# Kernel tuning notes

Measured on AMD Instinct MI355X. Metric: run time of the kernel, lower is better.

## Reference

```python
import jax, jax.numpy as jnp
import numpy as np

EPS = float(np.finfo(np.float64).eps)  # np.finfo(float).eps as in torch combine


def setup_inputs() -> dict:
    key = jax.random.key(0)
    ks = jax.random.split(key, 4)
    B, E, D_in, D_h, D_out = 4096, 8, 768, 2048, 768
    return {
        "x": jax.random.normal(ks[0], (B, D_in), dtype=jnp.float32),
        "w_gate": jax.random.normal(ks[1], (D_in, E), dtype=jnp.float32) * 0.02,
        "W1": jax.random.normal(ks[2], (E, D_in, D_h), dtype=jnp.float32) * (1.0 / np.sqrt(D_in)),
        "b1": jnp.zeros((E, D_h), dtype=jnp.float32),
        "W2": jax.random.normal(ks[3], (E, D_h, D_out), dtype=jnp.float32) * (1.0 / np.sqrt(D_h)),
        "b2": jnp.zeros((E, D_out), dtype=jnp.float32),
        "k": 2,
    }


def _cv_squared(v):
    # torch .var() is unbiased (ddof=1)
    return jnp.var(v, ddof=1) / (jnp.mean(v) ** 2 + 1e-10)


def _top_k_gates(logits, k):
    B, E = logits.shape
    top_vals, top_idx = jax.lax.top_k(logits, k)        # [B, k]
    top_gates = jax.nn.softmax(top_vals, axis=1)        # softmax over the k kept logits
    gates = jnp.zeros((B, E), logits.dtype).at[jnp.arange(B)[:, None], top_idx].set(top_gates)
    return gates


def reference(x, w_gate, W1, b1, W2, b2, k):
    # --- gating (eval path: noiseless clean logits, softmax gating) ---
    logits = x @ w_gate                                  # [B, E]
    gates = _top_k_gates(logits, k)                      # [B, E], sparse (k nonzeros/row)
    # --- per-expert MLP: Linear -> gelu -> Linear -> log_softmax ---
    # Dense grouped compute over experts; gate==0 terms contribute nothing in combine.
    h = jax.nn.gelu(jnp.einsum('bi,eih->beh', x, W1) + b1[None])      # [B, E, Dh]
    lo = jax.nn.log_softmax(jnp.einsum('beh,eho->beo', h, W2) + b2[None], axis=-1)  # [B, E, Do]
    # --- combine: exp, weight by gates, scatter-add, eps-clamp, log ---
    combined = jnp.einsum('be,beo->bo', gates, jnp.exp(lo))           # [B, Do]
    y = jnp.log(jnp.where(combined == 0, EPS, combined))
    # --- load-balancing aux loss (eval: load = count of nonzero gates) ---
    importance = gates.sum(0)
    load = (gates > 0).sum(0).astype(jnp.float32)
    loss = 0.01 * (_cv_squared(importance) + _cv_squared(load))
    return y, loss
```

## Files before the change

### kernel.cpp

```cpp
#include <hip/hip_runtime.h>
#include <hip/hip_bf16.h>
#include <math.h>

typedef __hip_bfloat16 bf16;
typedef short v8s __attribute__((ext_vector_type(8)));
typedef float v4f __attribute__((ext_vector_type(4)));

#define B_TOK 4096
#define E_EXP 8
#define D_IN  768
#define D_H   2048
#define D_OUT 768
#define MAXT  72

__device__ __forceinline__ void gl_lds16(const bf16* g, bf16* l) {
  __builtin_amdgcn_global_load_lds(
      (const __attribute__((address_space(1))) unsigned int*)g,
      (__attribute__((address_space(3))) unsigned int*)l, 16, 0, 0);
}

__global__ __launch_bounds__(256)
void prep_kernel(const float* __restrict__ x, const float* __restrict__ wg,
                 const float* __restrict__ W1, const float* __restrict__ W2,
                 bf16* __restrict__ W1t, bf16* __restrict__ W2t,
                 bf16* __restrict__ xb, float* __restrict__ gates,
                 int* __restrict__ tidx) {
  __shared__ bf16 tile[64][72];
  const int b = blockIdx.x;
  const int t = threadIdx.x;
  if (b < 6144) {
    const float* W; bf16* Wt; int K, N, kb, nb, e;
    if (b < 3072) {
      W = W1; Wt = W1t; K = D_IN; N = D_H;
      e = b / 384; int rem = b % 384; kb = rem % 12; nb = rem / 12;
    } else {
      int c = b - 3072;
      W = W2; Wt = W2t; K = D_H; N = D_OUT;
      e = c / 384; int rem = c % 384; kb = rem % 32; nb = rem / 32;
    }
    const int k0 = kb * 64, n0 = nb * 64;
    const int w = t >> 6, l = t & 63;
    const int a = l & 3, kl = l >> 2;
    const float* Wp = W + (size_t)e * K * N;
    #pragma unroll
    for (int p = 0; p < 4; ++p) {
      int k_loc = p * 16 + kl;
      int nb4 = w * 16 + a * 4;
      float4 v = *(const float4*)(Wp + (size_t)(k0 + k_loc) * N + n0 + nb4);
      float vv[4] = {v.x, v.y, v.z, v.w};
      #pragma unroll
      for (int i = 0; i < 4; ++i) {
        int n_loc = nb4 + i;
        int phys = (k_loc >> 3) ^ ((n_loc >> 2) & 7);
        tile[n_loc][phys * 8 + (k_loc & 7)] = __float2bfloat16(vv[i]);
      }
    }
    __syncthreads();
    bf16* Wtp = Wt + (size_t)e * N * K;
    const int nsub = l >> 2;
    #pragma unroll
    for (int p2 = 0; p2 < 2; ++p2) {
      int c = (l & 3) + p2 * 4;
      int n_loc = w * 16 + nsub;
      int phys = c ^ ((n_loc >> 2) & 7);
      v8s val = *(const v8s*)&tile[n_loc][phys * 8];
      *(v8s*)(Wtp + (size_t)(n0 + n_loc) * K + k0 + c * 8) = val;
    }
  } else {
    int gt = (b - 6144) * 256 + t;
    int tok = gt >> 6, l = gt & 63;
    const float* xr = x + (size_t)tok * D_IN;
    bf16* xbr = xb + (size_t)tok * D_IN;
    float acc[8] = {0.f,0.f,0.f,0.f,0.f,0.f,0.f,0.f};
    #pragma unroll
    for (int i = 0; i < 3; ++i) {
      int k0 = i * 256 + l * 4;
      float4 v = *(const float4*)(xr + k0);
      union { bf16 h[4]; uint2 u; } pk;
      pk.h[0] = __float2bfloat16(v.x); pk.h[1] = __float2bfloat16(v.y);
      pk.h[2] = __float2bfloat16(v.z); pk.h[3] = __float2bfloat16(v.w);
      *(uint2*)(xbr + k0) = pk.u;
      float xv[4] = {v.x, v.y, v.z, v.w};
      #pragma unroll
      for (int j = 0; j < 4; ++j) {
        const float* wr = wg + (size_t)(k0 + j) * 8;
        float4 w0 = *(const float4*)wr;
        float4 w1 = *(const float4*)(wr + 4);
        acc[0] += xv[j] * w0.x; acc[1] += xv[j] * w0.y;
        acc[2] += xv[j] * w0.z; acc[3] += xv[j] * w0.w;
        acc[4] += xv[j] * w1.x; acc[5] += xv[j] * w1.y;
        acc[6] += xv[j] * w1.z; acc[7] += xv[j] * w1.w;
      }
    }
    #pragma unroll
    for (int d = 1; d < 64; d <<= 1)
      #pragma unroll
      for (int e = 0; e < 8; ++e) acc[e] += __shfl_xor(acc[e], d);
    if (l == 0) {
      int i1 = 0; float v1 = acc[0];
      #pragma unroll
      for (int e = 1; e < 8; ++e) if (acc[e] > v1) { v1 = acc[e]; i1 = e; }
      int i2 = -1; float v2 = -1e30f;
      #pragma unroll
      for (int e = 0; e < 8; ++e) if (e != i1 && acc[e] > v2) { v2 = acc[e]; i2 = e; }
      float ex = __expf(v2 - v1);
      float g1 = 1.f / (1.f + ex), g2 = ex / (1.f + ex);
      gates[2 * tok] = g1; gates[2 * tok + 1] = g2;
      tidx[2 * tok] = i1;  tidx[2 * tok + 1] = i2;
    }
  }
}

__global__ void finalize_kernel(const int* __restrict__ tidx, const float* __restrict__ gates,
                                int* __restrict__ cnt_off, int* __restrict__ row_ids,
                                int* __restrict__ pos, int* __restrict__ tmap,
                                float* __restrict__ loss_out) {
  __shared__ int   hcnt[256][9];
  __shared__ float himp[256][9];
  __shared__ int   tot[8], off[8];
  __shared__ float itot[8];
  int t = threadIdx.x;
  #pragma unroll
  for (int e = 0; e < 8; ++e) { hcnt[t][e] = 0; himp[t][e] = 0.f; }
  __syncthreads();
  for (int i = 0; i < 32; ++i) {
    int idx = t * 32 + i;
    int e = tidx[idx];
    hcnt[t][e] += 1;
    himp[t][e] += gates[idx];
  }
  __syncthreads();
  if (t < 8) {
    int run = 0; float s = 0.f;
    for (int j = 0; j < 256; ++j) {
      int c = hcnt[j][t];
      hcnt[j][t] = run;
      run += c;
      s += himp[j][t];
    }
    tot[t] = run; itot[t] = s;
  }
  __syncthreads();
  if (t == 0) {
    int o = 0;
    float mi = 0.f, ml = 0.f;
    for (int e = 0; e < 8; ++e) {
      off[e] = o; o += tot[e];
      cnt_off[e] = tot[e]; cnt_off[8 + e] = off[e];
      mi += itot[e]; ml += (float)tot[e];
    }
    mi *= 0.125f; ml *= 0.125f;
    float vi = 0.f, vl = 0.f;
    for (int e = 0; e < 8; ++e) {
      float d = itot[e] - mi;        vi += d * d;
      float d2 = (float)tot[e] - ml; vl += d2 * d2;
    }
    vi /= 7.f; vl /= 7.f;
    *loss_out = 0.01f * (vi / (mi * mi + 1e-10f) + vl / (ml * ml + 1e-10f));
    int nt = 0;
    for (int e = 0; e < 8; ++e)
      for (int tt = 0; tt < (tot[e] + 127) >> 7; ++tt) {
        tmap[nt] = e; tmap[MAXT + nt] = tt; ++nt;
      }
    for (; nt < MAXT; ++nt) tmap[nt] = -1;
  }
  __syncthreads();
  for (int i = 0; i < 32; ++i) {
    int idx = t * 32 + i;
    int e = tidx[idx];
    int slot = off[e] + hcnt[t][e];
    hcnt[t][e] += 1;
    row_ids[slot] = idx >> 1;
    pos[idx] = slot;
  }
}

template<int KDIM, bool GATHER, bool GELU>
__global__ __launch_bounds__(256, 3)
void gemm_bk32(const bf16* __restrict__ Ab, const bf16* __restrict__ Wt,
               const float* __restrict__ bias, bf16* __restrict__ Outb,
               const int* __restrict__ row_ids, const int* __restrict__ cnt_off,
               const int* __restrict__ tmap, const int N) {
  constexpr int BK = 32, BM = 128, BN = 128;
  constexpr int NK = KDIM / BK;
  static_assert(NK % 2 == 0 && NK >= 4, "NK even, >=4");
  __shared__ __align__(16) bf16 lds[2][(BM + BN) * BK];
  const int ti = blockIdx.y;
  const int e = tmap[ti];
  if (e < 0) return;
  const int rowb = tmap[MAXT + ti];
  const int cnt = cnt_off[e];
  const int off = cnt_off[8 + e];
  const int colb = blockIdx.x;
  const int t = (int)threadIdx.x, w = t >> 6, l = t & 63;
  const int cs = (l & 3) ^ ((l >> 3) & 3);
  const bf16* gA[2];
  const bf16* gB[2];
  #pragma unroll
  for (int it = 0; it < 2; ++it) {
    int rt = (it * 4 + w) * 16 + (l >> 2);
    int r = rowb * BM + rt;
    int rc = r < cnt ? r : cnt - 1;
    long arow = GATHER ? (long)row_ids[off + rc] : (long)(off + rc);
    gA[it] = Ab + arow * (long)KDIM + cs * 8;
    gB[it] = Wt + ((size_t)e * N + (size_t)colb * BN + rt) * KDIM + cs * 8;
  }
  v4f acc[4][4] = {};
  const int wm = w >> 1, wn = w & 1;

#define STAGE(b, k0) do {                                                   \
    _Pragma("unroll")                                                       \
    for (int it = 0; it < 2; ++it)                                          \
      gl_lds16(gA[it] + (k0), &lds[b][(it * 4 + w) * 512]);                 \
    _Pragma("unroll")                                                       \
    for (int it = 0; it < 2; ++it)                                          \
      gl_lds16(gB[it] + (k0), &lds[b][BM * BK + (it * 4 + w) * 512]);       \
  } while (0)

#define COMPUTE(b) do {                                                     \
    __builtin_amdgcn_s_setprio(1);                                          \
    v8s af[4], bfr[4];                                                      \
    const int p = (l >> 4) ^ ((l >> 1) & 3);                                \
    _Pragma("unroll")                                                       \
    for (int fm = 0; fm < 4; ++fm) {                                        \
      int row = wm * 64 + fm * 16 + (l & 15);                               \
      af[fm] = *(const v8s*)(&lds[b][0] + row * BK + p * 8);                \
    }                                                                       \
    _Pragma("unroll")                                                       \
    for (int fn = 0; fn < 4; ++fn) {                                        \
      int row = wn * 64 + fn * 16 + (l & 15);                               \
      bfr[fn] = *(const v8s*)(&lds[b][BM * BK] + row * BK + p * 8);         \
    }                                                                       \
    _Pragma("unroll")                                                       \
    for (int fm = 0; fm < 4; ++fm)                                          \
      _Pragma("unroll")                                                     \
      for (int fn = 0; fn < 4; ++fn)                                        \
        acc[fm][fn] = __builtin_amdgcn_mfma_f32_16x16x32_bf16(af[fm], bfr[fn], acc[fm][fn], 0, 0, 0); \
    __builtin_amdgcn_s_setprio(0);                                          \
  } while (0)

#define SB    __builtin_amdgcn_sched_barrier(0)
#define BARR  __builtin_amdgcn_s_barrier()
#define WAIT4 asm volatile("s_waitcnt vmcnt(4)" ::: "memory")
#define WAITZ asm volatile("s_waitcnt vmcnt(0)" ::: "memory")

  STAGE(0, 0);
  #pragma unroll 1
  for (int ks = 0; ks < NK - 2; ks += 2) {
    STAGE(1, (ks + 1) * BK);
    WAIT4; SB; BARR; SB;
    COMPUTE(0);
    BARR; SB;
    STAGE(0, (ks + 2) * BK);
    WAIT4; SB; BARR; SB;
    COMPUTE(1);
    BARR; SB;
  }
  STAGE(1, (NK - 1) * BK);
  WAIT4; SB; BARR; SB;
  COMPUTE(0);
  WAITZ; SB; BARR; SB;
  COMPUTE(1);
  BARR; SB;
#undef STAGE
#undef COMPUTE
#undef WAIT4
#undef WAITZ

  float* eps = (float*)(&lds[0][0]) + w * (16 * 68);
  const float* bp = bias + (size_t)e * N + (size_t)colb * BN + wn * 64 + (l & 7) * 8;
  float bv[8];
  #pragma unroll
  for (int jj = 0; jj < 8; ++jj) bv[jj] = bp[jj];
  #pragma unroll
  for (int fm = 0; fm < 4; ++fm) {
    #pragma unroll
    for (int fn = 0; fn < 4; ++fn)
      #pragma unroll
      for (int q = 0; q < 4; ++q)
        eps[((l >> 4) * 4 + q) * 68 + fn * 16 + (l & 15)] = acc[fm][fn][q];
    #pragma unroll
    for (int half = 0; half < 2; ++half) {
      int row = (l >> 3) + 8 * half;
      int r = rowb * BM + wm * 64 + fm * 16 + row;
      if (r < cnt) {
        const float* rp = eps + row * 68 + (l & 7) * 8;
        union { bf16 h[8]; uint4 u; } pk;
        #pragma unroll
        for (int jj = 0; jj < 8; ++jj) {
          float v = rp[jj] + bv[jj];
          if (GELU) {
            float u = 0.7978845608028654f * (v + 0.044715f * v * v * v);
            float th = 1.f - 2.f / (__expf(2.f * u) + 1.f);
            v = 0.5f * v * (1.f + th);
          }
          pk.h[jj] = __float2bfloat16(v);
        }
        *(uint4*)(Outb + (size_t)(off + r) * N + (size_t)colb * BN + wn * 64 + (l & 7) * 8) = pk.u;
      }
    }
  }
#undef SB
#undef BARR
}

__global__ void combine_kernel(const bf16* __restrict__ z, const float* __restrict__ gates,
                               const int* __restrict__ pos, float* __restrict__ y) {
  int gt = blockIdx.x * 256 + threadIdx.x;
  int tok = gt >> 6, l = gt & 63;
  if (tok >= B_TOK) return;
  const bf16* z1 = z + (size_t)pos[2 * tok] * D_OUT;
  const bf16* z2 = z + (size_t)pos[2 * tok + 1] * D_OUT;
  float g1 = gates[2 * tok], g2 = gates[2 * tok + 1];
  float a[12], b[12];
  float m1 = -1e30f, m2 = -1e30f;
  #pragma unroll
  for (int i = 0; i < 12; ++i) {
    a[i] = __bfloat162float(z1[l + 64 * i]);
    b[i] = __bfloat162float(z2[l + 64 * i]);
    m1 = fmaxf(m1, a[i]); m2 = fmaxf(m2, b[i]);
  }
  #pragma unroll
  for (int d = 1; d < 64; d <<= 1) {
    m1 = fmaxf(m1, __shfl_xor(m1, d));
    m2 = fmaxf(m2, __shfl_xor(m2, d));
  }
  float s1 = 0.f, s2 = 0.f;
  #pragma unroll
  for (int i = 0; i < 12; ++i) { s1 += __expf(a[i] - m1); s2 += __expf(b[i] - m2); }
  #pragma unroll
  for (int d = 1; d < 64; d <<= 1) { s1 += __shfl_xor(s1, d); s2 += __shfl_xor(s2, d); }
  float c1 = g1 / s1, c2 = g2 / s2;
  #pragma unroll
  for (int i = 0; i < 12; ++i) {
    float cmb = c1 * __expf(a[i] - m1) + c2 * __expf(b[i] - m2);
    y[(size_t)tok * D_OUT + l + 64 * i] = logf(cmb == 0.f ? 2.2204460492503131e-16f : cmb);
  }
}

extern "C" void kernel_launch(void* const* d_in, const int* in_sizes, int n_in,
                              void* d_out, int out_size, void* d_ws, size_t ws_size,
                              hipStream_t stream) {
  const float* x  = (const float*)d_in[0];
  const float* wg = (const float*)d_in[1];
  const float* W1 = (const float*)d_in[2];
  const float* b1 = (const float*)d_in[3];
  const float* W2 = (const float*)d_in[4];
  const float* b2 = (const float*)d_in[5];
  float* out = (float*)d_out;

  char* ws = (char*)d_ws;
  int*   cnt_off = (int*)(ws + 0);
  float* gates   = (float*)(ws + 256);
  int*   tidx    = (int*)(ws + 256 + 32768);
  int*   pos     = (int*)(ws + 256 + 65536);
  int*   row_ids = (int*)(ws + 256 + 98304);
  int*   tmap    = (int*)(ws + 256 + 131072);
  const size_t base = 262144;
  bf16* x_bf = (bf16*)(ws + base);
  bf16* W1t  = (bf16*)(ws + base + 6291456);
  bf16* W2t  = (bf16*)(ws + base + 31457280);
  bf16* h_bf = (bf16*)(ws + base + 56623104);
  bf16* z_bf = (bf16*)(ws + base);

  prep_kernel<<<dim3(7168), 256, 0, stream>>>(x, wg, W1, W2, W1t, W2t, x_bf, gates, tidx);
  finalize_kernel<<<dim3(1), 256, 0, stream>>>(tidx, gates, cnt_off, row_ids, pos, tmap,
                                               out + (size_t)B_TOK * D_OUT);
  gemm_bk32<D_IN, true,  true ><<<dim3(D_H / 128, MAXT), 256, 0, stream>>>(
      x_bf, W1t, b1, h_bf, row_ids, cnt_off, tmap, D_H);
  gemm_bk32<D_H,  false, false><<<dim3(D_OUT / 128, MAXT), 256, 0, stream>>>(
      h_bf, W2t, b2, z_bf, row_ids, cnt_off, tmap, D_OUT);
  combine_kernel<<<dim3(1024), 256, 0, stream>>>(z_bf, gates, pos, out);
}
```

Before: 164.4 us.

## Move W2 transpose into first GEMM launch as extra blocks

Removes the W2 fp32-to-bf16 transpose from the prep kernel and runs it as 768 extra blocks (48 grid rows) appended to the first expert GEMM launch. Each extra block does four 64x64 tile transposes using the GEMM's shared memory. The idea is to overlap the W2 conversion with the W1 GEMM and shorten the serial prep kernel. The transpose tile load pattern is also reindexed. The cost is that these bandwidth-bound blocks now compete with GEMM blocks for CUs within the same launch.

```diff
diff --git a/kernel.cpp b/kernel.cpp
--- a/kernel.cpp
+++ b/kernel.cpp
@@ -19,55 +19,51 @@
       (__attribute__((address_space(3))) unsigned int*)l, 16, 0, 0);
 }
 
+__device__ __forceinline__ void transpose_tile64(
+    const float* __restrict__ W, bf16* __restrict__ Wt,
+    int K, int N, int e, int k0, int n0, int t, bf16 (*tile)[72]) {
+  const int w = t >> 6, l = t & 63;
+  const float* Wp = W + (size_t)e * K * N;
+  #pragma unroll
+  for (int p = 0; p < 4; ++p) {
+    int k_loc = w * 16 + p * 4 + (l >> 4);
+    int nn = (l & 15) * 4;
+    float4 v = *(const float4*)(Wp + (size_t)(k0 + k_loc) * N + n0 + nn);
+    float vv[4] = {v.x, v.y, v.z, v.w};
+    #pragma unroll
+    for (int i = 0; i < 4; ++i) {
+      int n_loc = nn + i;
+      int phys = (k_loc >> 3) ^ ((n_loc >> 2) & 7);
+      tile[n_loc][phys * 8 + (k_loc & 7)] = __float2bfloat16(vv[i]);
+    }
+  }
+  __syncthreads();
+  bf16* Wtp = Wt + (size_t)e * N * K;
+  const int nsub = l >> 2;
+  #pragma unroll
+  for (int p2 = 0; p2 < 2; ++p2) {
+    int c = (l & 3) + p2 * 4;
+    int n_loc = w * 16 + nsub;
+    int phys = c ^ ((n_loc >> 2) & 7);
+    v8s val = *(const v8s*)&tile[n_loc][phys * 8];
+    *(v8s*)(Wtp + (size_t)(n0 + n_loc) * K + k0 + c * 8) = val;
+  }
+}
+
 __global__ __launch_bounds__(256)
 void prep_kernel(const float* __restrict__ x, const float* __restrict__ wg,
-                 const float* __restrict__ W1, const float* __restrict__ W2,
-                 bf16* __restrict__ W1t, bf16* __restrict__ W2t,
+                 const float* __restrict__ W1, bf16* __restrict__ W1t,
                  bf16* __restrict__ xb, float* __restrict__ gates,
                  int* __restrict__ tidx) {
   __shared__ bf16 tile[64][72];
   const int b = blockIdx.x;
   const int t = threadIdx.x;
-  if (b < 6144) {
-    const float* W; bf16* Wt; int K, N, kb, nb, e;
-    if (b < 3072) {
-      W = W1; Wt = W1t; K = D_IN; N = D_H;
-      e = b / 384; int rem = b % 384; kb = rem % 12; nb = rem / 12;
-    } else {
-      int c = b - 3072;
-      W = W2; Wt = W2t; K = D_H; N = D_OUT;
-      e = c / 384; int rem = c % 384; kb = rem % 32; nb = rem / 32;
-    }
-    const int k0 = kb * 64, n0 = nb * 64;
-    const int w = t >> 6, l = t & 63;
-    const int a = l & 3, kl = l >> 2;
-    const float* Wp = W + (size_t)e * K * N;
-    #pragma unroll
-    for (int p = 0; p < 4; ++p) {
-      int k_loc = p * 16 + kl;
-      int nb4 = w * 16 + a * 4;
-      float4 v = *(const float4*)(Wp + (size_t)(k0 + k_loc) * N + n0 + nb4);
-      float vv[4] = {v.x, v.y, v.z, v.w};
-      #pragma unroll
-      for (int i = 0; i < 4; ++i) {
-        int n_loc = nb4 + i;
-        int phys = (k_loc >> 3) ^ ((n_loc >> 2) & 7);
-        tile[n_loc][phys * 8 + (k_loc & 7)] = __float2bfloat16(vv[i]);
-      }
-    }
-    __syncthreads();
-    bf16* Wtp = Wt + (size_t)e * N * K;
-    const int nsub = l >> 2;
-    #pragma unroll
-    for (int p2 = 0; p2 < 2; ++p2) {
-      int c = (l & 3) + p2 * 4;
-      int n_loc = w * 16 + nsub;
-      int phys = c ^ ((n_loc >> 2) & 7);
-      v8s val = *(const v8s*)&tile[n_loc][phys * 8];
-      *(v8s*)(Wtp + (size_t)(n0 + n_loc) * K + k0 + c * 8) = val;
-    }
+  if (b < 3072) {
+    int e = b / 384, rem = b % 384;
+    int kb = rem % 12, nb = rem / 12;
+    transpose_tile64(W1, W1t, D_IN, D_H, e, kb * 64, nb * 64, t, tile);
   } else {
-    int gt = (b - 6144) * 256 + t;
+    int gt = (b - 3072) * 256 + t;
     int tok = gt >> 6, l = gt & 63;
     const float* xr = x + (size_t)tok * D_IN;
     bf16* xbr = xb + (size_t)tok * D_IN;
@@ -95,14 +91,14 @@
     #pragma unroll
     for (int d = 1; d < 64; d <<= 1)
       #pragma unroll
-      for (int e = 0; e < 8; ++e) acc[e] += __shfl_xor(acc[e], d);
+      for (int e2 = 0; e2 < 8; ++e2) acc[e2] += __shfl_xor(acc[e2], d);
     if (l == 0) {
       int i1 = 0; float v1 = acc[0];
       #pragma unroll
-      for (int e = 1; e < 8; ++e) if (acc[e] > v1) { v1 = acc[e]; i1 = e; }
+      for (int e2 = 1; e2 < 8; ++e2) if (acc[e2] > v1) { v1 = acc[e2]; i1 = e2; }
       int i2 = -1; float v2 = -1e30f;
       #pragma unroll
-      for (int e = 0; e < 8; ++e) if (e != i1 && acc[e] > v2) { v2 = acc[e]; i2 = e; }
+      for (int e2 = 0; e2 < 8; ++e2) if (e2 != i1 && acc[e2] > v2) { v2 = acc[e2]; i2 = e2; }
       float ex = __expf(v2 - v1);
       float g1 = 1.f / (1.f + ex), g2 = ex / (1.f + ex);
       gates[2 * tok] = g1; gates[2 * tok + 1] = g2;
@@ -175,16 +171,30 @@
   }
 }
 
-template<int KDIM, bool GATHER, bool GELU>
+template<int KDIM, bool GATHER, bool GELU, bool DOTRANS>
 __global__ __launch_bounds__(256, 3)
 void gemm_bk32(const bf16* __restrict__ Ab, const bf16* __restrict__ Wt,
                const float* __restrict__ bias, bf16* __restrict__ Outb,
                const int* __restrict__ row_ids, const int* __restrict__ cnt_off,
-               const int* __restrict__ tmap, const int N) {
+               const int* __restrict__ tmap, const int N,
+               const float* __restrict__ Wsrc, bf16* __restrict__ Wdst) {
   constexpr int BK = 32, BM = 128, BN = 128;
   constexpr int NK = KDIM / BK;
   static_assert(NK % 2 == 0 && NK >= 4, "NK even, >=4");
   __shared__ __align__(16) bf16 lds[2][(BM + BN) * BK];
+  const int t = (int)threadIdx.x, w = t >> 6, l = t & 63;
+  if (DOTRANS && blockIdx.y >= MAXT) {
+    int tid = (blockIdx.y - MAXT) * gridDim.x + blockIdx.x;
+    int e = tid / 96, r = tid % 96;
+    int kb = r % 8, nb = r / 8;
+    bf16 (*tile)[72] = (bf16(*)[72])&lds[0][0];
+    #pragma unroll 1
+    for (int sub = 0; sub < 4; ++sub) {
+      transpose_tile64(Wsrc, Wdst, D_H, D_OUT, e, kb * 256 + sub * 64, nb * 64, t, tile);
+      __syncthreads();
+    }
+    return;
+  }
   const int ti = blockIdx.y;
   const int e = tmap[ti];
   if (e < 0) return;
@@ -192,7 +202,6 @@
   const int cnt = cnt_off[e];
   const int off = cnt_off[8 + e];
   const int colb = blockIdx.x;
-  const int t = (int)threadIdx.x, w = t >> 6, l = t & 63;
   const int cs = (l & 3) ^ ((l >> 3) & 3);
   const bf16* gA[2];
   const bf16* gB[2];
@@ -363,12 +372,12 @@
   bf16* h_bf = (bf16*)(ws + base + 56623104);
   bf16* z_bf = (bf16*)(ws + base);
 
-  prep_kernel<<<dim3(7168), 256, 0, stream>>>(x, wg, W1, W2, W1t, W2t, x_bf, gates, tidx);
+  prep_kernel<<<dim3(4096), 256, 0, stream>>>(x, wg, W1, W1t, x_bf, gates, tidx);
   finalize_kernel<<<dim3(1), 256, 0, stream>>>(tidx, gates, cnt_off, row_ids, pos, tmap,
                                                out + (size_t)B_TOK * D_OUT);
-  gemm_bk32<D_IN, true,  true ><<<dim3(D_H / 128, MAXT), 256, 0, stream>>>(
-      x_bf, W1t, b1, h_bf, row_ids, cnt_off, tmap, D_H);
-  gemm_bk32<D_H,  false, false><<<dim3(D_OUT / 128, MAXT), 256, 0, stream>>>(
-      h_bf, W2t, b2, z_bf, row_ids, cnt_off, tmap, D_OUT);
+  gemm_bk32<D_IN, true,  true,  true ><<<dim3(D_H / 128, MAXT + 48), 256, 0, stream>>>(
+      x_bf, W1t, b1, h_bf, row_ids, cnt_off, tmap, D_H, W2, W2t);
+  gemm_bk32<D_H,  false, false, false><<<dim3(D_OUT / 128, MAXT), 256, 0, stream>>>(
+      h_bf, W2t, b2, z_bf, row_ids, cnt_off, tmap, D_OUT, nullptr, nullptr);
   combine_kernel<<<dim3(1024), 256, 0, stream>>>(z_bf, gates, pos, out);
 }
```

Measured after the change: 159.5 us. 1.03x faster.
